# Kernel tuning notes

Hardware: AMD Instinct MI355X
Metric: run time of the kernel (lower is better)

The kernel has to match this reference:

```python
import jax, jax.numpy as jnp
import numpy as np

N = 500000
V = 50000
GF = 64
OC = 256

def _lin(key, din, dout):
    k1, k2 = jax.random.split(key)
    w = jax.random.normal(k1, (din, dout), dtype=jnp.float32) * 0.02
    b = jax.random.normal(k2, (dout,), dtype=jnp.float32) * 0.02
    return w, b

def setup_inputs() -> dict:
    key = jax.random.key(0)
    ks = jax.random.split(key, 12)
    inp_feat = jax.random.normal(ks[0], (N, 6), dtype=jnp.float32)
    vox2point_idx = jax.random.randint(ks[1], (N,), 0, V, dtype=jnp.int32)
    w1x, b1x = _lin(ks[2], 3, GF)
    w2x, b2x = _lin(ks[3], GF, OC // 8)
    w1r, b1r = _lin(ks[4], 3, GF)
    w2r, b2r = _lin(ks[5], GF, OC // 8)
    wax, bax = _lin(ks[6], OC // 4, OC // 8)
    war, bar = _lin(ks[7], OC // 4, OC // 8)
    wv1, bv1 = _lin(ks[8], OC // 2, OC // 2)
    w3, b3 = _lin(ks[9], OC, OC)
    w4, b4 = _lin(ks[10], OC, OC)
    wv2, bv2 = _lin(ks[11], OC, OC)
    return dict(inp_feat=inp_feat, vox2point_idx=vox2point_idx, num_vox=V,
                w1x=w1x, b1x=b1x, w2x=w2x, b2x=b2x,
                w1r=w1r, b1r=b1r, w2r=w2r, b2r=b2r,
                wax=wax, bax=bax, war=war, bar=bar,
                wv1=wv1, bv1=bv1, w3=w3, b3=b3, w4=w4, b4=b4,
                wv2=wv2, bv2=bv2)

def reference(inp_feat, vox2point_idx, num_vox,
              w1x, b1x, w2x, b2x, w1r, b1r, w2r, b2r,
              wax, bax, war, bar, wv1, bv1, w3, b3, w4, b4, wv2, bv2):
    relu = jax.nn.relu
    xyz = inp_feat[:, :3]
    rgb = inp_feat[:, 3:]
    fx = relu(relu(xyz @ w1x + b1x) @ w2x + b2x)   # [N, 32]
    fr = relu(relu(rgb @ w1r + b1r) @ w2r + b2r)   # [N, 32]
    comb = jnp.concatenate([fx, fr], axis=-1)       # [N, 64]
    pf2 = jnp.concatenate([
        fx, fx * jax.nn.sigmoid(comb @ wax + bax),
        fr, fr * jax.nn.sigmoid(comb @ war + bar)], axis=-1)  # [N, 128]
    # scatter-max to voxels; torch_scatter fills empty segments with 0 and
    # pf2 >= 0 elementwise, so clamp -inf (jax empty fill) to 0 for parity.
    vox = jax.ops.segment_max(pf2, vox2point_idx, num_segments=num_vox)
    vox = jnp.maximum(vox, 0.0)                     # [V, 128]
    vox = relu(vox @ wv1 + bv1)
    pg = vox[vox2point_idx]                          # gather back [N, 128]
    pf3 = jnp.concatenate([pg, pf2], axis=-1)        # [N, 256]
    pf5 = relu(relu(pf3 @ w3 + b3) @ w4 + b4)        # [N, 256]
    vox2 = jax.ops.segment_max(pf5, vox2point_idx, num_segments=num_vox)
    vox2 = jnp.maximum(vox2, 0.0)
    return relu(vox2 @ wv2 + bv2)                    # [V, 256]
```

## Files before the change

kernel.cpp:

```cpp
#include <hip/hip_runtime.h>

#define NPTS 500000
#define NVOX 50000
#define NBLK 196

typedef unsigned short u16;
typedef unsigned int u32;
typedef __attribute__((ext_vector_type(8))) short short8;
typedef __attribute__((ext_vector_type(4))) float floatx4;
typedef __attribute__((ext_vector_type(4))) unsigned int uintx4;
typedef __attribute__((ext_vector_type(2))) unsigned int uintx2;

__device__ __forceinline__ u16 f2bf(float f) {
    u32 u = __float_as_uint(f);
    u = u + 0x7fffu + ((u >> 16) & 1u);
    return (u16)(u >> 16);
}

#if defined(__has_builtin)
#if __has_builtin(__builtin_amdgcn_cvt_pk_bf16_f32)
#define HAVE_PKBF 1
#endif
#endif

__device__ __forceinline__ u32 pkbf(float a, float b) {
#ifdef HAVE_PKBF
    typedef __attribute__((ext_vector_type(2))) __bf16 bf16x2;
    bf16x2 v = __builtin_amdgcn_cvt_pk_bf16_f32(a, b);
    u32 r; __builtin_memcpy(&r, &v, 4);
    return r;
#else
    return (u32)f2bf(a) | ((u32)f2bf(b) << 16);
#endif
}

__device__ __forceinline__ void wswz(const float* __restrict__ W, u16* __restrict__ Wf, int N, int t) {
    int k = t / N, n = t - k * N;
    int kk = k >> 5, q = (k >> 3) & 3, j = k & 7;
    Wf[((size_t)((kk * 4 + q) * N + n) << 3) + j] = f2bf(W[t]);
}

__global__ __launch_bounds__(256) void k_wprep(
    const float* __restrict__ w3, const float* __restrict__ w4,
    const float* __restrict__ wv1, const float* __restrict__ wv2,
    const float* __restrict__ w2x, const float* __restrict__ w2r,
    const float* __restrict__ wax, const float* __restrict__ war,
    const float* __restrict__ w1x, const float* __restrict__ b1x,
    const float* __restrict__ w1r, const float* __restrict__ b1r,
    u16* __restrict__ w3f, u16* __restrict__ w4f, u16* __restrict__ wv1f, u16* __restrict__ wv2f,
    u16* __restrict__ wcatf, u16* __restrict__ wattf, u16* __restrict__ w1ef)
{
    int t = blockIdx.x * 256 + threadIdx.x;
    if (t < 65536) { wswz(w3, w3f, 256, t); return; }  t -= 65536;
    if (t < 65536) { wswz(w4, w4f, 256, t); return; }  t -= 65536;
    if (t < 65536) { wswz(wv2, wv2f, 256, t); return; } t -= 65536;
    if (t < 16384) { wswz(wv1, wv1f, 128, t); return; } t -= 16384;
    if (t < 8192) {
        int k = t >> 6, n = t & 63;
        float v;
        if (k < 64) v = (n < 32) ? w2x[k * 32 + n] : 0.f;
        else        v = (n >= 32) ? w2r[(k - 64) * 32 + (n - 32)] : 0.f;
        int kk = k >> 5, q = (k >> 3) & 3, j = k & 7;
        wcatf[((size_t)((kk * 4 + q) * 64 + n) << 3) + j] = f2bf(v);
        return;
    }
    t -= 8192;
    if (t < 4096) {
        int k = t >> 6, n = t & 63;
        float v = (n < 32) ? wax[k * 32 + n] : war[k * 32 + (n - 32)];
        int kk = k >> 5, q = (k >> 3) & 3, j = k & 7;
        wattf[((size_t)((kk * 4 + q) * 64 + n) << 3) + j] = f2bf(v);
        return;
    }
    t -= 4096;
    if (t < 4096) {
        int k = t >> 7, n = t & 127;
        float v = 0.f;
        if (n < 64) {
            if (k < 3)       v = w1x[k * 64 + n];
            else if (k == 3) v = b1x[n];
        } else {
            if (k >= 4 && k < 7) v = w1r[(k - 4) * 64 + (n - 64)];
            else if (k == 7)     v = b1r[n - 64];
        }
        int q = (k >> 3) & 3, j = k & 7;
        w1ef[((size_t)(q * 128 + n) << 3) + j] = f2bf(v);
    }
}

__global__ void k_hist(const int* __restrict__ idx, int* __restrict__ hcnt) {
    int i = blockIdx.x * 256 + threadIdx.x;
    if (i < NPTS) atomicAdd(&hcnt[idx[i]], 1);
}

__global__ __launch_bounds__(256) void k_scan1(const int* __restrict__ hcnt, int* __restrict__ bsum) {
    __shared__ int wsum[4];
    int t = threadIdx.x;
    int i = blockIdx.x * 256 + t;
    int c = (i < NVOX) ? hcnt[i] : 0;
    #pragma unroll
    for (int d = 32; d >= 1; d >>= 1) c += __shfl_xor(c, d, 64);
    if ((t & 63) == 0) wsum[t >> 6] = c;
    __syncthreads();
    if (t == 0) bsum[blockIdx.x] = wsum[0] + wsum[1] + wsum[2] + wsum[3];
}

__global__ __launch_bounds__(256) void k_scan2(const int* __restrict__ bsum, int* __restrict__ boff) {
    __shared__ int wsum[4];
    int t = threadIdx.x, lane = t & 63, w = t >> 6;
    int c = (t < NBLK) ? bsum[t] : 0;
    int v = c;
    #pragma unroll
    for (int d = 1; d < 64; d <<= 1) {
        int o = __shfl_up(v, d, 64);
        if (lane >= d) v += o;
    }
    if (lane == 63) wsum[w] = v;
    __syncthreads();
    int wo = 0;
    #pragma unroll
    for (int k = 0; k < 4; k++) if (k < w) wo += wsum[k];
    if (t < NBLK) boff[t] = wo + v - c;
}

__global__ __launch_bounds__(256) void k_scan3(const int* __restrict__ hcnt, const int* __restrict__ boff,
                                               int* __restrict__ cur) {
    __shared__ int wsum[4];
    int t = threadIdx.x, lane = t & 63, w = t >> 6;
    int i = blockIdx.x * 256 + t;
    int c = (i < NVOX) ? hcnt[i] : 0;
    int v = c;
    #pragma unroll
    for (int d = 1; d < 64; d <<= 1) {
        int o = __shfl_up(v, d, 64);
        if (lane >= d) v += o;
    }
    if (lane == 63) wsum[w] = v;
    __syncthreads();
    int wo = 0;
    #pragma unroll
    for (int k = 0; k < 4; k++) if (k < w) wo += wsum[k];
    if (i < NVOX) cur[i] = boff[blockIdx.x] + wo + v - c;
}

__global__ void k_scatter(const int* __restrict__ idx, int* __restrict__ cur,
                          int* __restrict__ sptid, int* __restrict__ svid) {
    int i = blockIdx.x * 256 + threadIdx.x;
    if (i < NPTS) {
        int v = idx[i];
        int pos = atomicAdd(&cur[v], 1);
        sptid[pos] = i;
        svid[pos] = v;
    }
}

__global__ __launch_bounds__(256) void k_pointfeat(
    const float* __restrict__ inp, const int* __restrict__ sptid, const int* __restrict__ svid,
    const u16* __restrict__ w1ef,
    const u16* __restrict__ wcatf, const float* __restrict__ b2x, const float* __restrict__ b2r,
    const u16* __restrict__ wattf, const float* __restrict__ bax, const float* __restrict__ bar,
    u16* __restrict__ pf2s, float* __restrict__ voxmax)
{
    __shared__ u16 hbuf[64 * 136];
    __shared__ u16 cbuf[64 * 72];
    __shared__ u16 abuf[64 * 40];
    __shared__ int lvid[64];
    int t = threadIdx.x;
    int i0 = blockIdx.x * 64;
    int mcnt = NPTS - i0; if (mcnt > 64) mcnt = 64;
    if (t < 64) lvid[t] = (t < mcnt) ? svid[i0 + t] : -1;
    {
        int m = t >> 2, c = t & 3;
        u16* ab = &abuf[m * 40];
        bool act = (m < mcnt);
        if (c < 3) {
            float2 v = {0.f, 0.f};
            if (act) v = *(const float2*)(inp + (size_t)sptid[i0 + m] * 6 + 2 * c);
            if (c == 0)      { ab[0] = f2bf(v.x); ab[1] = f2bf(v.y); }
            else if (c == 1) { ab[2] = f2bf(v.x); ab[4] = f2bf(v.y); }
            else             { ab[5] = f2bf(v.x); ab[6] = f2bf(v.y); }
        } else {
            u16 one = act ? (u16)0x3F80 : (u16)0;
            ab[3] = one; ab[7] = one;
        }
        #pragma unroll
        for (int z = 0; z < 3; z++) *(u32*)&ab[8 + 6 * c + 2 * z] = 0;
    }
    __syncthreads();
    int wave = t >> 6, l = t & 63, q = l >> 4, lm = l & 15;
    {
        floatx4 hacc[4][2];
        #pragma unroll
        for (int a = 0; a < 4; a++)
            #pragma unroll
            for (int b = 0; b < 2; b++) hacc[a][b] = (floatx4){0.f, 0.f, 0.f, 0.f};
        short8 bfrag[2], afrag[4];
        #pragma unroll
        for (int tn = 0; tn < 2; tn++)
            bfrag[tn] = *(const short8*)&w1ef[(size_t)(q * 128 + wave * 32 + tn * 16 + lm) * 8];
        #pragma unroll
        for (int tm = 0; tm < 4; tm++)
            afrag[tm] = *(const short8*)&abuf[(tm * 16 + lm) * 40 + q * 8];
        #pragma unroll
        for (int tm = 0; tm < 4; tm++)
            #pragma unroll
            for (int tn = 0; tn < 2; tn++)
                hacc[tm][tn] = __builtin_amdgcn_mfma_f32_16x16x32_bf16(afrag[tm], bfrag[tn], hacc[tm][tn], 0, 0, 0);
        #pragma unroll
        for (int tm = 0; tm < 4; tm++)
            #pragma unroll
            for (int tn = 0; tn < 2; tn++) {
                int n2 = wave * 32 + tn * 16 + lm;
                #pragma unroll
                for (int r = 0; r < 4; r++) {
                    int m = tm * 16 + q * 4 + r;
                    hbuf[m * 136 + n2] = f2bf(fmaxf(hacc[tm][tn][r], 0.f));
                }
            }
    }
    __syncthreads();
    int n = wave * 16 + lm;
    floatx4 acc[4];
    #pragma unroll
    for (int a = 0; a < 4; a++) acc[a] = (floatx4){0.f, 0.f, 0.f, 0.f};
    #pragma unroll
    for (int kk = 0; kk < 4; kk++) {
        short8 bfrag = *(const short8*)&wcatf[(size_t)((kk * 4 + q) * 64 + n) << 3];
        #pragma unroll
        for (int tm = 0; tm < 4; tm++) {
            short8 afrag = *(const short8*)&hbuf[(tm * 16 + lm) * 136 + kk * 32 + q * 8];
            acc[tm] = __builtin_amdgcn_mfma_f32_16x16x32_bf16(afrag, bfrag, acc[tm], 0, 0, 0);
        }
    }
    float bv = (n < 32) ? b2x[n] : b2r[n - 32];
    float comb_keep[4][4];
    #pragma unroll
    for (int tm = 0; tm < 4; tm++)
        #pragma unroll
        for (int r = 0; r < 4; r++) {
            float v = fmaxf(acc[tm][r] + bv, 0.f);
            comb_keep[tm][r] = v;
            int m = tm * 16 + q * 4 + r;
            cbuf[m * 72 + n] = f2bf(v);
        }
    __syncthreads();
    floatx4 acc2[4];
    #pragma unroll
    for (int a = 0; a < 4; a++) acc2[a] = (floatx4){0.f, 0.f, 0.f, 0.f};
    #pragma unroll
    for (int kk = 0; kk < 2; kk++) {
        short8 bfrag = *(const short8*)&wattf[(size_t)((kk * 4 + q) * 64 + n) << 3];
        #pragma unroll
        for (int tm = 0; tm < 4; tm++) {
            short8 afrag = *(const short8*)&cbuf[(tm * 16 + lm) * 72 + kk * 32 + q * 8];
            acc2[tm] = __builtin_amdgcn_mfma_f32_16x16x32_bf16(afrag, bfrag, acc2[tm], 0, 0, 0);
        }
    }
    float bv2 = (n < 32) ? bax[n] : bar[n - 32];
    int pp = (n < 32) ? n : 32 + n;
    #pragma unroll
    for (int tm = 0; tm < 4; tm++)
        #pragma unroll
        for (int r = 0; r < 4; r++) {
            float att = acc2[tm][r] + bv2;
            float sg = 1.f / (1.f + __expf(-att));
            float plain = comb_keep[tm][r];
            float gated = plain * sg;
            int m = tm * 16 + q * 4 + r;
            hbuf[m * 136 + pp] = f2bf(plain);
            hbuf[m * 136 + pp + 32] = f2bf(gated);
        }
    __syncthreads();
    {
        int row = t >> 2, seg = t & 3;
        if (row < mcnt) {
            const u16* src = &hbuf[row * 136 + seg * 32];
            u16* dst = pf2s + (size_t)(i0 + row) * 128 + seg * 32;
            *(uintx4*)dst = *(const uintx4*)src;
            *(uintx4*)(dst + 8) = *(const uintx4*)(src + 8);
        }
    }
    {
        int c2 = t & 63;
        int h = t >> 6;
        int r0 = h * 16;
        int r1 = r0 + 16; if (r1 > mcnt) r1 = mcnt;
        u32 mlo = 0, mhi = 0;
        int pvid = -1;
        for (int r = r0; r < r1; r++) {
            int vid = lvid[r];
            if (vid != pvid) {
                if (pvid >= 0) {
                    int* addr = (int*)(voxmax + (size_t)pvid * 128 + 2 * c2);
                    if (mlo) atomicMax(addr, (int)mlo);
                    if (mhi) atomicMax(addr + 1, (int)mhi);
                }
                pvid = vid; mlo = 0; mhi = 0;
            }
            u32 u = *(const u32*)&hbuf[r * 136 + 2 * c2];
            u32 lo = u << 16, hi = u & 0xffff0000u;
            mlo = lo > mlo ? lo : mlo;
            mhi = hi > mhi ? hi : mhi;
        }
        if (pvid >= 0) {
            int* addr = (int*)(voxmax + (size_t)pvid * 128 + 2 * c2);
            if (mlo) atomicMax(addr, (int)mlo);
            if (mhi) atomicMax(addr + 1, (int)mhi);
        }
    }
}

template<int K, int N, bool ABF16, bool OUT_BF16>
__global__ __launch_bounds__(256) void k_gemm_relu(
    const void* __restrict__ Ap, const u16* __restrict__ Wf,
    const float* __restrict__ bias, void* __restrict__ outp, int M)
{
    constexpr int STRIDE = K + 8;
    constexpr int TN = N / 64;
    constexpr int KSTEPS = K / 32;
    constexpr int CW = K / 4;
    __shared__ u16 lds[64 * STRIDE];
    int i0 = blockIdx.x * 64;
    int mcnt = M - i0; if (mcnt > 64) mcnt = 64;
    int t = threadIdx.x;
    {
        int row = t >> 2, cseg = t & 3;
        u16* dst = &lds[row * STRIDE + cseg * CW];
        if (row < mcnt) {
            if (ABF16) {
                const u16* src = (const u16*)Ap + (size_t)(i0 + row) * K + cseg * CW;
                #pragma unroll
                for (int c = 0; c < CW / 8; c++)
                    *(uintx4*)(dst + c * 8) = *(const uintx4*)(src + c * 8);
            } else {
                const float* src = (const float*)Ap + (size_t)(i0 + row) * K + cseg * CW;
                #pragma unroll
                for (int c = 0; c < CW / 8; c++) {
                    float4 v0 = *(const float4*)(src + c * 8);
                    float4 v1 = *(const float4*)(src + c * 8 + 4);
                    uintx4 rr = {pkbf(v0.x, v0.y), pkbf(v0.z, v0.w), pkbf(v1.x, v1.y), pkbf(v1.z, v1.w)};
                    *(uintx4*)(dst + c * 8) = rr;
                }
            }
        } else {
            uintx4 z = {0, 0, 0, 0};
            #pragma unroll
            for (int c = 0; c < CW / 8; c++) *(uintx4*)(dst + c * 8) = z;
        }
    }
    __syncthreads();
    int wave = t >> 6, l = t & 63;
    int q = l >> 4, lm = l & 15;
    int wn0 = wave * (N / 4);
    floatx4 acc[4][TN];
    #pragma unroll
    for (int a = 0; a < 4; a++)
        #pragma unroll
        for (int b = 0; b < TN; b++) acc[a][b] = (floatx4){0.f, 0.f, 0.f, 0.f};
    #pragma unroll
    for (int kk = 0; kk < KSTEPS; kk++) {
        short8 afrag[4], bfrag[TN];
        #pragma unroll
        for (int tm = 0; tm < 4; tm++)
            afrag[tm] = *(const short8*)&lds[(tm * 16 + lm) * STRIDE + kk * 32 + q * 8];
        #pragma unroll
        for (int tn = 0; tn < TN; tn++)
            bfrag[tn] = *(const short8*)&Wf[(size_t)((kk * 4 + q) * N + wn0 + tn * 16 + lm) * 8];
        #pragma unroll
        for (int tm = 0; tm < 4; tm++)
            #pragma unroll
            for (int tn = 0; tn < TN; tn++)
                acc[tm][tn] = __builtin_amdgcn_mfma_f32_16x16x32_bf16(afrag[tm], bfrag[tn], acc[tm][tn], 0, 0, 0);
    }
    #pragma unroll
    for (int tm = 0; tm < 4; tm++)
        #pragma unroll
        for (int tn = 0; tn < TN; tn++) {
            int n = wn0 + tn * 16 + lm;
            float bv = bias[n];
            #pragma unroll
            for (int r = 0; r < 4; r++) {
                int m = tm * 16 + q * 4 + r;
                if (m < mcnt) {
                    float v = fmaxf(acc[tm][tn][r] + bv, 0.f);
                    if (OUT_BF16) ((u16*)outp)[(size_t)(i0 + m) * N + n] = f2bf(v);
                    else          ((float*)outp)[(size_t)(i0 + m) * N + n] = v;
                }
            }
        }
}

__global__ __launch_bounds__(256) void k_pointmlp(
    const u16* __restrict__ voxf, const u16* __restrict__ pf2s, const int* __restrict__ svid,
    const u16* __restrict__ w3f, const float* __restrict__ b3,
    const u16* __restrict__ w4f, const float* __restrict__ b4,
    float* __restrict__ vox2)
{
    constexpr int STRIDE = 264;
    __shared__ u16 lds[64 * STRIDE];
    __shared__ int lvid[64];
    __shared__ float bl[512];
    int i0 = blockIdx.x * 64;
    int mcnt = NPTS - i0; if (mcnt > 64) mcnt = 64;
    int t = threadIdx.x;
    if (t < 64) lvid[t] = (t < mcnt) ? svid[i0 + t] : -1;
    for (int s = t; s < 512; s += 256) bl[s] = (s < 256) ? b3[s] : b4[s - 256];
    {
        int row = t >> 2, cseg = t & 3;
        u16* dst = &lds[row * STRIDE + cseg * 64];
        if (row < mcnt) {
            const u16* src;
            if (cseg < 2) src = voxf + (size_t)svid[i0 + row] * 128 + cseg * 64;
            else          src = pf2s + (size_t)(i0 + row) * 128 + (cseg - 2) * 64;
            #pragma unroll
            for (int c = 0; c < 8; c++)
                *(uintx4*)(dst + c * 8) = *(const uintx4*)(src + c * 8);
        } else {
            uintx4 z = {0, 0, 0, 0};
            #pragma unroll
            for (int c = 0; c < 8; c++) *(uintx4*)(dst + c * 8) = z;
        }
    }
    __syncthreads();
    int wave = t >> 6, l = t & 63;
    int q = l >> 4, lm = l & 15;
    int wm0 = wave * 64;
    floatx4 acc[4][4];
    #pragma unroll
    for (int a = 0; a < 4; a++)
        #pragma unroll
        for (int b = 0; b < 4; b++) acc[a][b] = (floatx4){0.f, 0.f, 0.f, 0.f};
    #pragma unroll
    for (int kk = 0; kk < 8; kk++) {
        short8 wfrag[4], bfrag[4];
        #pragma unroll
        for (int tm = 0; tm < 4; tm++)
            wfrag[tm] = *(const short8*)&w3f[(size_t)((kk * 4 + q) * 256 + wm0 + tm * 16 + lm) * 8];
        #pragma unroll
        for (int tn = 0; tn < 4; tn++)
            bfrag[tn] = *(const short8*)&lds[(tn * 16 + lm) * STRIDE + kk * 32 + q * 8];
        #pragma unroll
        for (int tm = 0; tm < 4; tm++)
            #pragma unroll
            for (int tn = 0; tn < 4; tn++)
                acc[tm][tn] = __builtin_amdgcn_mfma_f32_16x16x32_bf16(wfrag[tm], bfrag[tn], acc[tm][tn], 0, 0, 0);
    }
    __syncthreads();
    #pragma unroll
    for (int tm = 0; tm < 4; tm++) {
        float4 bq = *(const float4*)&bl[wm0 + tm * 16 + 4 * q];
        #pragma unroll
        for (int tn = 0; tn < 4; tn++) {
            u32 lo = pkbf(fmaxf(acc[tm][tn][0] + bq.x, 0.f), fmaxf(acc[tm][tn][1] + bq.y, 0.f));
            u32 hi = pkbf(fmaxf(acc[tm][tn][2] + bq.z, 0.f), fmaxf(acc[tm][tn][3] + bq.w, 0.f));
            *(uintx2*)&lds[(tn * 16 + lm) * STRIDE + wm0 + tm * 16 + 4 * q] = (uintx2){lo, hi};
        }
    }
    __syncthreads();
    floatx4 acc2[4][4];
    #pragma unroll
    for (int a = 0; a < 4; a++)
        #pragma unroll
        for (int b = 0; b < 4; b++) acc2[a][b] = (floatx4){0.f, 0.f, 0.f, 0.f};
    #pragma unroll
    for (int kk = 0; kk < 8; kk++) {
        short8 wfrag[4], bfrag[4];
        #pragma unroll
        for (int tm = 0; tm < 4; tm++)
            wfrag[tm] = *(const short8*)&w4f[(size_t)((kk * 4 + q) * 256 + wm0 + tm * 16 + lm) * 8];
        #pragma unroll
        for (int tn = 0; tn < 4; tn++)
            bfrag[tn] = *(const short8*)&lds[(tn * 16 + lm) * STRIDE + kk * 32 + q * 8];
        #pragma unroll
        for (int tm = 0; tm < 4; tm++)
            #pragma unroll
            for (int tn = 0; tn < 4; tn++)
                acc2[tm][tn] = __builtin_amdgcn_mfma_f32_16x16x32_bf16(wfrag[tm], bfrag[tn], acc2[tm][tn], 0, 0, 0);
    }
    __syncthreads();
    #pragma unroll
    for (int tm = 0; tm < 4; tm++) {
        float4 bq = *(const float4*)&bl[256 + wm0 + tm * 16 + 4 * q];
        #pragma unroll
        for (int tn = 0; tn < 4; tn++) {
            u32 lo = pkbf(fmaxf(acc2[tm][tn][0] + bq.x, 0.f), fmaxf(acc2[tm][tn][1] + bq.y, 0.f));
            u32 hi = pkbf(fmaxf(acc2[tm][tn][2] + bq.z, 0.f), fmaxf(acc2[tm][tn][3] + bq.w, 0.f));
            *(uintx2*)&lds[(tn * 16 + lm) * STRIDE + wm0 + tm * 16 + 4 * q] = (uintx2){lo, hi};
        }
    }
    __syncthreads();
    {
        int c4 = t & 63;
        int g = t >> 6;
        int r0 = g * 16;
        int r1 = r0 + 16; if (r1 > mcnt) r1 = mcnt;
        u32 m0 = 0, m1 = 0, m2 = 0, m3 = 0;
        int pvid = -1;
        for (int r = r0; r < r1; r++) {
            int vid = lvid[r];
            if (vid != pvid) {
                if (pvid >= 0) {
                    int* addr = (int*)(vox2 + (size_t)pvid * 256 + 4 * c4);
                    if (m0) atomicMax(addr,     (int)m0);
                    if (m1) atomicMax(addr + 1, (int)m1);
                    if (m2) atomicMax(addr + 2, (int)m2);
                    if (m3) atomicMax(addr + 3, (int)m3);
                }
                pvid = vid; m0 = m1 = m2 = m3 = 0;
            }
            uintx2 u = *(const uintx2*)&lds[r * STRIDE + 4 * c4];
            u32 a0 = u[0] << 16, a1 = u[0] & 0xffff0000u;
            u32 a2 = u[1] << 16, a3 = u[1] & 0xffff0000u;
            m0 = a0 > m0 ? a0 : m0;
            m1 = a1 > m1 ? a1 : m1;
            m2 = a2 > m2 ? a2 : m2;
            m3 = a3 > m3 ? a3 : m3;
        }
        if (pvid >= 0) {
            int* addr = (int*)(vox2 + (size_t)pvid * 256 + 4 * c4);
            if (m0) atomicMax(addr,     (int)m0);
            if (m1) atomicMax(addr + 1, (int)m1);
            if (m2) atomicMax(addr + 2, (int)m2);
            if (m3) atomicMax(addr + 3, (int)m3);
        }
    }
}

extern "C" void kernel_launch(void* const* d_in, const int* in_sizes, int n_in,
                              void* d_out, int out_size, void* d_ws, size_t ws_size,
                              hipStream_t stream) {
    const float* inp = (const float*)d_in[0];
    const int*   idx = (const int*)d_in[1];
    const float* w1x = (const float*)d_in[3];  const float* b1x = (const float*)d_in[4];
    const float* w2x = (const float*)d_in[5];  const float* b2x = (const float*)d_in[6];
    const float* w1r = (const float*)d_in[7];  const float* b1r = (const float*)d_in[8];
    const float* w2r = (const float*)d_in[9];  const float* b2r = (const float*)d_in[10];
    const float* wax = (const float*)d_in[11]; const float* bax = (const float*)d_in[12];
    const float* war = (const float*)d_in[13]; const float* bar = (const float*)d_in[14];
    const float* wv1 = (const float*)d_in[15]; const float* bv1 = (const float*)d_in[16];
    const float* w3  = (const float*)d_in[17]; const float* b3  = (const float*)d_in[18];
    const float* w4  = (const float*)d_in[19]; const float* b4  = (const float*)d_in[20];
    const float* wv2 = (const float*)d_in[21]; const float* bv2 = (const float*)d_in[22];
    float* out = (float*)d_out;

    char* ws = (char*)d_ws;
    u16*   pf2s   = (u16*)ws;   ws += (size_t)NPTS * 128 * sizeof(u16);
    float* voxmax = (float*)ws; ws += (size_t)NVOX * 128 * sizeof(float);
    u16*   voxf   = (u16*)ws;   ws += (size_t)NVOX * 128 * sizeof(u16);
    float* vox2   = (float*)ws; ws += (size_t)NVOX * 256 * sizeof(float);
    u16*   w3f    = (u16*)ws;   ws += 65536 * sizeof(u16);
    u16*   w4f    = (u16*)ws;   ws += 65536 * sizeof(u16);
    u16*   wv1f   = (u16*)ws;   ws += 16384 * sizeof(u16);
    u16*   wv2f   = (u16*)ws;   ws += 65536 * sizeof(u16);
    u16*   wcatf  = (u16*)ws;   ws += 8192 * sizeof(u16);
    u16*   wattf  = (u16*)ws;   ws += 4096 * sizeof(u16);
    u16*   w1ef   = (u16*)ws;   ws += 4096 * sizeof(u16);
    int*   hcnt   = (int*)ws;   ws += (size_t)NVOX * sizeof(int);
    int*   cur    = (int*)ws;   ws += (size_t)NVOX * sizeof(int);
    int*   bsum   = (int*)ws;   ws += (size_t)NBLK * sizeof(int);
    int*   boff   = (int*)ws;   ws += (size_t)NBLK * sizeof(int);
    int*   sptid  = (int*)ws;   ws += (size_t)NPTS * sizeof(int);
    int*   svid   = (int*)ws;   ws += (size_t)NPTS * sizeof(int);

    hipMemsetAsync(hcnt, 0, (size_t)NVOX * sizeof(int), stream);
    hipMemsetAsync(voxmax, 0, (size_t)NVOX * 128 * sizeof(float), stream);
    hipMemsetAsync(vox2, 0, (size_t)NVOX * 256 * sizeof(float), stream);

    k_wprep<<<896, 256, 0, stream>>>(w3, w4, wv1, wv2, w2x, w2r, wax, war,
                                     w1x, b1x, w1r, b1r,
                                     w3f, w4f, wv1f, wv2f, wcatf, wattf, w1ef);

    k_hist<<<(NPTS + 255) / 256, 256, 0, stream>>>(idx, hcnt);
    k_scan1<<<NBLK, 256, 0, stream>>>(hcnt, bsum);
    k_scan2<<<1, 256, 0, stream>>>(bsum, boff);
    k_scan3<<<NBLK, 256, 0, stream>>>(hcnt, boff, cur);
    k_scatter<<<(NPTS + 255) / 256, 256, 0, stream>>>(idx, cur, sptid, svid);

    k_pointfeat<<<(NPTS + 63) / 64, 256, 0, stream>>>(
        inp, sptid, svid, w1ef, wcatf, b2x, b2r, wattf, bax, bar, pf2s, voxmax);

    k_gemm_relu<128, 128, false, true><<<(NVOX + 63) / 64, 256, 0, stream>>>(
        (const void*)voxmax, wv1f, bv1, (void*)voxf, NVOX);

    k_pointmlp<<<(NPTS + 63) / 64, 256, 0, stream>>>(
        voxf, pf2s, svid, w3f, b3, w4f, b4, vox2);

    k_gemm_relu<256, 256, false, false><<<(NVOX + 63) / 64, 256, 0, stream>>>(
        (const void*)vox2, wv2f, bv2, (void*)out, NVOX);
}
```

Before: 545.9 us.

## Transpose pointfeat MFMAs to weight-as-A and vectorize packed LDS stores

Swaps the MFMA operand roles in the point-feature kernel so weights are the A operand and points the B operand. Each lane then holds four consecutive channels and can write packed bf16 pairs as 64-bit LDS stores instead of scattered 16-bit stores. Biases are staged in shared memory and read as float4. The scatter-max loops now compare 16-bit values and shift them when issuing atomics, and the second scatter uses 128 columns by 32 rows per thread instead of 64 by 16. This is meant to cut LDS store traffic and bank conflicts, and trades fewer, wider atomic streams per thread for a different access pattern.

```diff
diff --git a/kernel.cpp b/kernel.cpp
--- a/kernel.cpp
+++ b/kernel.cpp
@@ -164,11 +164,14 @@
     __shared__ u16 hbuf[64 * 136];
     __shared__ u16 cbuf[64 * 72];
     __shared__ u16 abuf[64 * 40];
+    __shared__ float bl[128];
     __shared__ int lvid[64];
     int t = threadIdx.x;
     int i0 = blockIdx.x * 64;
     int mcnt = NPTS - i0; if (mcnt > 64) mcnt = 64;
     if (t < 64) lvid[t] = (t < mcnt) ? svid[i0 + t] : -1;
+    else if (t < 128) { int s = t - 64;  bl[s] = (s < 32) ? b2x[s] : b2r[s - 32]; }
+    else if (t < 192) { int s = t - 128; bl[64 + s] = (s < 32) ? bax[s] : bar[s - 32]; }
     {
         int m = t >> 2, c = t & 3;
         u16* ab = &abuf[m * 40];
@@ -189,87 +192,87 @@
     __syncthreads();
     int wave = t >> 6, l = t & 63, q = l >> 4, lm = l & 15;
     {
-        floatx4 hacc[4][2];
-        #pragma unroll
-        for (int a = 0; a < 4; a++)
-            #pragma unroll
-            for (int b = 0; b < 2; b++) hacc[a][b] = (floatx4){0.f, 0.f, 0.f, 0.f};
-        short8 bfrag[2], afrag[4];
-        #pragma unroll
-        for (int tn = 0; tn < 2; tn++)
-            bfrag[tn] = *(const short8*)&w1ef[(size_t)(q * 128 + wave * 32 + tn * 16 + lm) * 8];
-        #pragma unroll
-        for (int tm = 0; tm < 4; tm++)
-            afrag[tm] = *(const short8*)&abuf[(tm * 16 + lm) * 40 + q * 8];
-        #pragma unroll
-        for (int tm = 0; tm < 4; tm++)
-            #pragma unroll
-            for (int tn = 0; tn < 2; tn++)
-                hacc[tm][tn] = __builtin_amdgcn_mfma_f32_16x16x32_bf16(afrag[tm], bfrag[tn], hacc[tm][tn], 0, 0, 0);
-        #pragma unroll
-        for (int tm = 0; tm < 4; tm++)
-            #pragma unroll
-            for (int tn = 0; tn < 2; tn++) {
-                int n2 = wave * 32 + tn * 16 + lm;
-                #pragma unroll
-                for (int r = 0; r < 4; r++) {
-                    int m = tm * 16 + q * 4 + r;
-                    hbuf[m * 136 + n2] = f2bf(fmaxf(hacc[tm][tn][r], 0.f));
-                }
+        floatx4 hacc[2][4];
+        #pragma unroll
+        for (int a = 0; a < 2; a++)
+            #pragma unroll
+            for (int b = 0; b < 4; b++) hacc[a][b] = (floatx4){0.f, 0.f, 0.f, 0.f};
+        short8 wfrag[2], bfrag[4];
+        #pragma unroll
+        for (int tm = 0; tm < 2; tm++)
+            wfrag[tm] = *(const short8*)&w1ef[(size_t)(q * 128 + wave * 32 + tm * 16 + lm) * 8];
+        #pragma unroll
+        for (int tn = 0; tn < 4; tn++)
+            bfrag[tn] = *(const short8*)&abuf[(tn * 16 + lm) * 40 + q * 8];
+        #pragma unroll
+        for (int tm = 0; tm < 2; tm++)
+            #pragma unroll
+            for (int tn = 0; tn < 4; tn++)
+                hacc[tm][tn] = __builtin_amdgcn_mfma_f32_16x16x32_bf16(wfrag[tm], bfrag[tn], hacc[tm][tn], 0, 0, 0);
+        #pragma unroll
+        for (int tm = 0; tm < 2; tm++) {
+            int ch0 = wave * 32 + tm * 16 + 4 * q;
+            #pragma unroll
+            for (int tn = 0; tn < 4; tn++) {
+                int pt = tn * 16 + lm;
+                u32 lo = pkbf(fmaxf(hacc[tm][tn][0], 0.f), fmaxf(hacc[tm][tn][1], 0.f));
+                u32 hi = pkbf(fmaxf(hacc[tm][tn][2], 0.f), fmaxf(hacc[tm][tn][3], 0.f));
+                *(uintx2*)&hbuf[pt * 136 + ch0] = (uintx2){lo, hi};
             }
-    }
-    __syncthreads();
-    int n = wave * 16 + lm;
+        }
+    }
+    __syncthreads();
     floatx4 acc[4];
     #pragma unroll
     for (int a = 0; a < 4; a++) acc[a] = (floatx4){0.f, 0.f, 0.f, 0.f};
     #pragma unroll
     for (int kk = 0; kk < 4; kk++) {
-        short8 bfrag = *(const short8*)&wcatf[(size_t)((kk * 4 + q) * 64 + n) << 3];
-        #pragma unroll
-        for (int tm = 0; tm < 4; tm++) {
-            short8 afrag = *(const short8*)&hbuf[(tm * 16 + lm) * 136 + kk * 32 + q * 8];
-            acc[tm] = __builtin_amdgcn_mfma_f32_16x16x32_bf16(afrag, bfrag, acc[tm], 0, 0, 0);
-        }
-    }
-    float bv = (n < 32) ? b2x[n] : b2r[n - 32];
+        short8 wfrag = *(const short8*)&wcatf[(size_t)((kk * 4 + q) * 64 + wave * 16 + lm) * 8];
+        #pragma unroll
+        for (int tn = 0; tn < 4; tn++) {
+            short8 bfrag = *(const short8*)&hbuf[(tn * 16 + lm) * 136 + kk * 32 + q * 8];
+            acc[tn] = __builtin_amdgcn_mfma_f32_16x16x32_bf16(wfrag, bfrag, acc[tn], 0, 0, 0);
+        }
+    }
+    int ch0 = wave * 16 + 4 * q;
+    float4 bq = *(const float4*)&bl[ch0];
     float comb_keep[4][4];
     #pragma unroll
-    for (int tm = 0; tm < 4; tm++)
-        #pragma unroll
-        for (int r = 0; r < 4; r++) {
-            float v = fmaxf(acc[tm][r] + bv, 0.f);
-            comb_keep[tm][r] = v;
-            int m = tm * 16 + q * 4 + r;
-            cbuf[m * 72 + n] = f2bf(v);
-        }
+    for (int tn = 0; tn < 4; tn++) {
+        int pt = tn * 16 + lm;
+        float c0 = fmaxf(acc[tn][0] + bq.x, 0.f);
+        float c1 = fmaxf(acc[tn][1] + bq.y, 0.f);
+        float c2 = fmaxf(acc[tn][2] + bq.z, 0.f);
+        float c3 = fmaxf(acc[tn][3] + bq.w, 0.f);
+        comb_keep[tn][0] = c0; comb_keep[tn][1] = c1; comb_keep[tn][2] = c2; comb_keep[tn][3] = c3;
+        *(uintx2*)&cbuf[pt * 72 + ch0] = (uintx2){pkbf(c0, c1), pkbf(c2, c3)};
+    }
     __syncthreads();
     floatx4 acc2[4];
     #pragma unroll
     for (int a = 0; a < 4; a++) acc2[a] = (floatx4){0.f, 0.f, 0.f, 0.f};
     #pragma unroll
     for (int kk = 0; kk < 2; kk++) {
-        short8 bfrag = *(const short8*)&wattf[(size_t)((kk * 4 + q) * 64 + n) << 3];
-        #pragma unroll
-        for (int tm = 0; tm < 4; tm++) {
-            short8 afrag = *(const short8*)&cbuf[(tm * 16 + lm) * 72 + kk * 32 + q * 8];
-            acc2[tm] = __builtin_amdgcn_mfma_f32_16x16x32_bf16(afrag, bfrag, acc2[tm], 0, 0, 0);
-        }
-    }
-    float bv2 = (n < 32) ? bax[n] : bar[n - 32];
-    int pp = (n < 32) ? n : 32 + n;
-    #pragma unroll
-    for (int tm = 0; tm < 4; tm++)
-        #pragma unroll
-        for (int r = 0; r < 4; r++) {
-            float att = acc2[tm][r] + bv2;
-            float sg = 1.f / (1.f + __expf(-att));
-            float plain = comb_keep[tm][r];
-            float gated = plain * sg;
-            int m = tm * 16 + q * 4 + r;
-            hbuf[m * 136 + pp] = f2bf(plain);
-            hbuf[m * 136 + pp + 32] = f2bf(gated);
-        }
+        short8 wfrag = *(const short8*)&wattf[(size_t)((kk * 4 + q) * 64 + wave * 16 + lm) * 8];
+        #pragma unroll
+        for (int tn = 0; tn < 4; tn++) {
+            short8 bfrag = *(const short8*)&cbuf[(tn * 16 + lm) * 72 + kk * 32 + q * 8];
+            acc2[tn] = __builtin_amdgcn_mfma_f32_16x16x32_bf16(wfrag, bfrag, acc2[tn], 0, 0, 0);
+        }
+    }
+    float4 bq2 = *(const float4*)&bl[64 + ch0];
+    int pp0 = (ch0 < 32) ? ch0 : 32 + ch0;
+    #pragma unroll
+    for (int tn = 0; tn < 4; tn++) {
+        int pt = tn * 16 + lm;
+        float s0 = 1.f / (1.f + __expf(-(acc2[tn][0] + bq2.x)));
+        float s1 = 1.f / (1.f + __expf(-(acc2[tn][1] + bq2.y)));
+        float s2 = 1.f / (1.f + __expf(-(acc2[tn][2] + bq2.z)));
+        float s3 = 1.f / (1.f + __expf(-(acc2[tn][3] + bq2.w)));
+        float p0 = comb_keep[tn][0], p1 = comb_keep[tn][1], p2 = comb_keep[tn][2], p3 = comb_keep[tn][3];
+        *(uintx2*)&hbuf[pt * 136 + pp0]      = (uintx2){pkbf(p0, p1), pkbf(p2, p3)};
+        *(uintx2*)&hbuf[pt * 136 + pp0 + 32] = (uintx2){pkbf(p0 * s0, p1 * s1), pkbf(p2 * s2, p3 * s3)};
+    }
     __syncthreads();
     {
         int row = t >> 2, seg = t & 3;
@@ -292,20 +295,20 @@
             if (vid != pvid) {
                 if (pvid >= 0) {
                     int* addr = (int*)(voxmax + (size_t)pvid * 128 + 2 * c2);
-                    if (mlo) atomicMax(addr, (int)mlo);
-                    if (mhi) atomicMax(addr + 1, (int)mhi);
+                    if (mlo) atomicMax(addr, (int)(mlo << 16));
+                    if (mhi) atomicMax(addr + 1, (int)(mhi << 16));
                 }
                 pvid = vid; mlo = 0; mhi = 0;
             }
             u32 u = *(const u32*)&hbuf[r * 136 + 2 * c2];
-            u32 lo = u << 16, hi = u & 0xffff0000u;
+            u32 lo = u & 0xffffu, hi = u >> 16;
             mlo = lo > mlo ? lo : mlo;
             mhi = hi > mhi ? hi : mhi;
         }
         if (pvid >= 0) {
             int* addr = (int*)(voxmax + (size_t)pvid * 128 + 2 * c2);
-            if (mlo) atomicMax(addr, (int)mlo);
-            if (mhi) atomicMax(addr + 1, (int)mhi);
+            if (mlo) atomicMax(addr, (int)(mlo << 16));
+            if (mhi) atomicMax(addr + 1, (int)(mhi << 16));
         }
     }
 }
@@ -490,38 +493,31 @@
     }
     __syncthreads();
     {
-        int c4 = t & 63;
-        int g = t >> 6;
-        int r0 = g * 16;
-        int r1 = r0 + 16; if (r1 > mcnt) r1 = mcnt;
-        u32 m0 = 0, m1 = 0, m2 = 0, m3 = 0;
+        int c2 = t & 127;
+        int h = t >> 7;
+        int r0 = h * 32;
+        int r1 = r0 + 32; if (r1 > mcnt) r1 = mcnt;
+        u32 mlo = 0, mhi = 0;
         int pvid = -1;
         for (int r = r0; r < r1; r++) {
             int vid = lvid[r];
             if (vid != pvid) {
                 if (pvid >= 0) {
-                    int* addr = (int*)(vox2 + (size_t)pvid * 256 + 4 * c4);
-                    if (m0) atomicMax(addr,     (int)m0);
-                    if (m1) atomicMax(addr + 1, (int)m1);
-                    if (m2) atomicMax(addr + 2, (int)m2);
-                    if (m3) atomicMax(addr + 3, (int)m3);
+                    int* addr = (int*)(vox2 + (size_t)pvid * 256 + 2 * c2);
+                    if (mlo) atomicMax(addr, (int)(mlo << 16));
+                    if (mhi) atomicMax(addr + 1, (int)(mhi << 16));
                 }
-                pvid = vid; m0 = m1 = m2 = m3 = 0;
+                pvid = vid; mlo = 0; mhi = 0;
             }
-            uintx2 u = *(const uintx2*)&lds[r * STRIDE + 4 * c4];
-            u32 a0 = u[0] << 16, a1 = u[0] & 0xffff0000u;
-            u32 a2 = u[1] << 16, a3 = u[1] & 0xffff0000u;
-            m0 = a0 > m0 ? a0 : m0;
-            m1 = a1 > m1 ? a1 : m1;
-            m2 = a2 > m2 ? a2 : m2;
-            m3 = a3 > m3 ? a3 : m3;
+            u32 u = *(const u32*)&lds[r * STRIDE + 2 * c2];
+            u32 lo = u & 0xffffu, hi = u >> 16;
+            mlo = lo > mlo ? lo : mlo;
+            mhi = hi > mhi ? hi : mhi;
         }
         if (pvid >= 0) {
-            int* addr = (int*)(vox2 + (size_t)pvid * 256 + 4 * c4);
-            if (m0) atomicMax(addr,     (int)m0);
-            if (m1) atomicMax(addr + 1, (int)m1);
-            if (m2) atomicMax(addr + 2, (int)m2);
-            if (m3) atomicMax(addr + 3, (int)m3);
+            int* addr = (int*)(vox2 + (size_t)pvid * 256 + 2 * c2);
+            if (mlo) atomicMax(addr, (int)(mlo << 16));
+            if (mhi) atomicMax(addr + 1, (int)(mhi << 16));
         }
     }
 }
```

Result: faster. 506.2 us (-7.3%).
